# Kernel tuning notes

Measured on AMD Instinct MI355X. Metric: run time of the kernel, lower is better.

## Reference

```python
import jax, jax.numpy as jnp
import numpy as np

D = 1024
H = 16
DH = D // H
B, T = 2, 2048


def setup_inputs() -> dict:
    key = jax.random.key(0)
    ks = jax.random.split(key, 5)
    x = jax.random.normal(ks[0], (B, T, D), dtype=jnp.float32)
    # torch nn.Linear init scale ~ 1/sqrt(fan_in)
    sc = 1.0 / np.sqrt(D)
    W_qkv = jax.random.uniform(ks[1], (3 * D, D), dtype=jnp.float32, minval=-sc, maxval=sc)
    b_qkv = jax.random.uniform(ks[2], (3 * D,), dtype=jnp.float32, minval=-sc, maxval=sc)
    W_o = jax.random.uniform(ks[3], (D, D), dtype=jnp.float32, minval=-sc, maxval=sc)
    b_o = jax.random.uniform(ks[4], (D,), dtype=jnp.float32, minval=-sc, maxval=sc)
    return {"x": x, "W_qkv": W_qkv, "b_qkv": b_qkv, "W_o": W_o, "b_o": b_o}


def reference(x, W_qkv, b_qkv, W_o, b_o):
    Bx, Tx, C = x.shape
    scale = DH ** -0.5
    qkv = x @ W_qkv.T + b_qkv                       # [B,T,3D]
    qkv = qkv.reshape(Bx, Tx, 3, H, DH)
    q, k, v = jnp.moveaxis(qkv, 2, 0)               # each [B,T,H,DH]
    q = q.transpose(0, 2, 1, 3)                     # [B,H,T,DH]
    k = k.transpose(0, 2, 1, 3)
    v = v.transpose(0, 2, 1, 3)
    scores = jnp.einsum("bhqd,bhkd->bhqk", q, k) * scale
    a = jax.nn.softmax(scores, axis=-1)
    o = jnp.einsum("bhqk,bhkd->bhqd", a, v)         # [B,H,T,DH]
    o = o.transpose(0, 2, 1, 3).reshape(Bx, Tx, C)
    return o @ W_o.T + b_o
```

## Files before the change

kernel.cpp:

```cpp
#include <hip/hip_runtime.h>

#define TT 2048
#define DD 1024
#define HH 16
#define DHH 64

typedef __attribute__((ext_vector_type(4)))  float  f32x4;
typedef __attribute__((ext_vector_type(16))) float  f32x16;
typedef __attribute__((ext_vector_type(8)))  short  bf16x8;
typedef __attribute__((ext_vector_type(4)))  float  f4;
typedef __attribute__((ext_vector_type(4)))  unsigned short u16x4;
typedef __attribute__((ext_vector_type(4)))  unsigned int   u32x4;

__device__ __forceinline__ unsigned short f2b(float f) {
    union { float f; unsigned int u; } v; v.f = f;
    unsigned int r = v.u + 0x7fffu + ((v.u >> 16) & 1u);
    return (unsigned short)(r >> 16);
}

__device__ __forceinline__ void gl_lds16(const void* g, void* l) {
    __builtin_amdgcn_global_load_lds(
        (const __attribute__((address_space(1))) unsigned int*)g,
        (__attribute__((address_space(3))) unsigned int*)l, 16, 0, 0);
}

__device__ __forceinline__ f32x16 mfma32(bf16x8 a, bf16x8 b, f32x16 c) {
    return __builtin_amdgcn_mfma_f32_32x32x16_bf16(a, b, c, 0, 0, 0);
}

__device__ __forceinline__ float fexp2(float x) {
    float r; asm("v_exp_f32 %0, %1" : "=v"(r) : "v"(x)); return r;
}

__device__ __forceinline__ unsigned int pkbf(float a, float b) {
    unsigned int r;
    asm("v_cvt_pk_bf16_f32 %0, %1, %2" : "=v"(r) : "v"(a), "v"(b));
    return r;
}

__device__ __forceinline__ void pl32swap(unsigned int& a, unsigned int& b) {
    asm("v_permlane32_swap_b32 %0, %1" : "+v"(a), "+v"(b));
}

__device__ __forceinline__ bf16x8 u2h(u32x4 u) {
    union { u32x4 u; bf16x8 h; } x; x.u = u; return x.h;
}

__global__ void f2b3_kernel(const float* __restrict__ x, const float* __restrict__ wq,
                            const float* __restrict__ wo, unsigned short* __restrict__ d) {
    int i = blockIdx.x * blockDim.x + threadIdx.x;
    const float* s; int off;
    if (i < 1048576)      { s = x;  off = i; }
    else if (i < 1835008) { s = wq; off = i - 1048576; }
    else                  { s = wo; off = i - 1835008; }
    f4 v = ((const f4*)s)[off];
    u16x4 o;
    o[0] = f2b(v[0]); o[1] = f2b(v[1]); o[2] = f2b(v[2]); o[3] = f2b(v[3]);
    ((u16x4*)d)[i] = o;
}

template<int BN, int MODE>
__global__ __launch_bounds__(256) void gemm_bt(
    const unsigned short* __restrict__ A, const unsigned short* __restrict__ Bm,
    const float* __restrict__ bias, int N, int K,
    unsigned short* __restrict__ q, unsigned short* __restrict__ k,
    unsigned short* __restrict__ vt, float* __restrict__ outf)
{
    constexpr int NB  = BN / 32;
    constexpr int ASZ = 128 * 32;
    constexpr int BSZ = BN * 32;
    __shared__ unsigned short lds[2 * (ASZ + BSZ)];

    int tid = threadIdx.x;
    int l = tid & 63, w = tid >> 6;
    int wr = w >> 1, wc = w & 1;
    int lr = l & 15, lk = (l >> 4) * 8;
    int bm = blockIdx.y, bn = blockIdx.x;

    f32x4 acc[4][NB] = {};

    const unsigned short* Ag = A + (size_t)(bm * 128) * K;
    const unsigned short* Bg = Bm + (size_t)(bn * BN) * K;

    auto stage = [&](int buf, int k0) {
        unsigned short* As = lds + buf * (ASZ + BSZ);
        unsigned short* Bs = As + ASZ;
#pragma unroll
        for (int r = 0; r < 2; ++r) {
            int e = r * 256 + tid;
            int row = e >> 2, kc = (e & 3) * 8;
            gl_lds16(Ag + (size_t)row * K + k0 + kc, &As[e * 8]);
        }
#pragma unroll
        for (int r = 0; r < BN / 64; ++r) {
            int e = r * 256 + tid;
            int row = e >> 2, kc = (e & 3) * 8;
            gl_lds16(Bg + (size_t)row * K + k0 + kc, &Bs[e * 8]);
        }
    };

    stage(0, 0);
    __syncthreads();
    int cur = 0;
    for (int k0 = 0; k0 < K; k0 += 32) {
        if (k0 + 32 < K) stage(cur ^ 1, k0 + 32);
        const unsigned short* As = lds + cur * (ASZ + BSZ);
        const unsigned short* Bs = As + ASZ;
        bf16x8 a[4], b[NB];
#pragma unroll
        for (int i = 0; i < 4; ++i)
            a[i] = *(const bf16x8*)&As[(wr * 64 + i * 16 + lr) * 32 + lk];
#pragma unroll
        for (int j = 0; j < NB; ++j)
            b[j] = *(const bf16x8*)&Bs[(wc * (BN / 2) + j * 16 + lr) * 32 + lk];
        __builtin_amdgcn_s_setprio(1);
#pragma unroll
        for (int i = 0; i < 4; ++i)
#pragma unroll
            for (int j = 0; j < NB; ++j)
                acc[i][j] = __builtin_amdgcn_mfma_f32_16x16x32_bf16(a[i], b[j], acc[i][j], 0, 0, 0);
        __builtin_amdgcn_s_setprio(0);
        __syncthreads();
        cur ^= 1;
    }

#pragma unroll
    for (int i = 0; i < 4; ++i) {
#pragma unroll
        for (int j = 0; j < NB; ++j) {
            int row0 = bm * 128 + wr * 64 + i * 16 + (l >> 4) * 4;
            int col  = bn * BN + wc * (BN / 2) + j * 16 + (l & 15);
            float bv = bias[col];
#pragma unroll
            for (int r = 0; r < 4; ++r) {
                float val = acc[i][j][r] + bv;
                int m = row0 + r;
                if (MODE == 0) {
                    int which = col >> 10, rem = col & 1023;
                    int h = rem >> 6, d = rem & 63;
                    int b = m >> 11, t = m & 2047;
                    if (which == 0) {
                        q[((size_t)((b * HH + h) * TT + t)) * DHH + d] = f2b(val * 0.18033688011112042f);
                    } else if (which == 1) {
                        k[((size_t)((b * HH + h) * TT + t)) * DHH + d] = f2b(val);
                    } else {
                        vt[((size_t)((b * HH + h) * DHH + d)) * TT + t] = f2b(val);
                    }
                } else {
                    outf[(size_t)m * N + col] = val;
                }
            }
        }
    }
}

__global__ __launch_bounds__(512, 4) void attn(
    const unsigned short* __restrict__ qb,
    const unsigned short* __restrict__ kb,
    const unsigned short* __restrict__ vtb,
    unsigned short* __restrict__ ob)
{
    extern __shared__ char lds[];

    int tid = threadIdx.x;
    int l = tid & 63, w = tid >> 6;
    int g = w >> 2, wg = w & 3;
    int hi = l >> 5, c = l & 31;
    int tig = tid & 255;

    int lin = blockIdx.x;
    int swz = (lin & 7) * 64 + (lin >> 3);
    int bh = swz >> 4;
    int qrow = (swz & 15) * 128 + wg * 32 + c;

    bf16x8 qf[4];
    const unsigned short* qg = qb + ((size_t)bh * TT + qrow) * DHH;
#pragma unroll
    for (int kd = 0; kd < 4; ++kd)
        qf[kd] = *(const bf16x8*)(qg + kd * 16 + hi * 8);

    f32x16 oa0 = {}, oa1 = {};
    float m = -1e30f, lsum = 0.f;

    const char* kgl = (const char*)(kb + (size_t)bh * TT * DHH) + (size_t)g * 1024 * 128;
    const char* vgl = (const char*)(vtb + (size_t)bh * DHH * TT) + (size_t)g * 1024 * 2;
    char* base = lds + g * 16384;

    for (int kt0 = 0; kt0 < 1024; kt0 += 64) {
#pragma unroll
        for (int r = 0; r < 2; ++r) {
            int p = r * 4096 + tig * 16;
            int rw = p >> 7, qq = p & 127;
            int sw = qq ^ ((rw & 7) << 4);
            gl_lds16(kgl + (size_t)(kt0 + rw) * 128 + sw, base + p);
            gl_lds16(vgl + (size_t)rw * (TT * 2) + kt0 * 2 + sw, base + 8192 + p);
        }
        __syncthreads();
        const char* Ksb = base;
        const char* Vsb = base + 8192;

        f32x16 s0 = {}, s1 = {};
        __builtin_amdgcn_s_setprio(1);
#pragma unroll
        for (int kd = 0; kd < 4; ++kd) {
            int cb = (kd * 16 + hi * 8) * 2;
            int xr = cb ^ ((c & 7) << 4);
            bf16x8 kf0 = *(const bf16x8*)(Ksb + c * 128 + xr);
            bf16x8 kf1 = *(const bf16x8*)(Ksb + (32 + c) * 128 + xr);
            s0 = mfma32(kf0, qf[kd], s0);
            s1 = mfma32(kf1, qf[kd], s1);
        }
        __builtin_amdgcn_s_setprio(0);

        float mx[11];
#pragma unroll
        for (int r = 0; r < 10; ++r)
            mx[r] = fmaxf(fmaxf(s0[3 * r], s0[3 * r + 1]), s0[3 * r + 2]);
        mx[0] = fmaxf(fmaxf(s0[0], s0[1]), s0[2]);
        mx[1] = fmaxf(fmaxf(s0[3], s0[4]), s0[5]);
        mx[2] = fmaxf(fmaxf(s0[6], s0[7]), s0[8]);
        mx[3] = fmaxf(fmaxf(s0[9], s0[10]), s0[11]);
        mx[4] = fmaxf(fmaxf(s0[12], s0[13]), s0[14]);
        mx[5] = fmaxf(fmaxf(s0[15], s1[0]), s1[1]);
        mx[6] = fmaxf(fmaxf(s1[2], s1[3]), s1[4]);
        mx[7] = fmaxf(fmaxf(s1[5], s1[6]), s1[7]);
        mx[8] = fmaxf(fmaxf(s1[8], s1[9]), s1[10]);
        mx[9] = fmaxf(fmaxf(s1[11], s1[12]), s1[13]);
        mx[10] = fmaxf(s1[14], s1[15]);
        float t0 = fmaxf(fmaxf(mx[0], mx[1]), mx[2]);
        float t1 = fmaxf(fmaxf(mx[3], mx[4]), mx[5]);
        float t2 = fmaxf(fmaxf(mx[6], mx[7]), mx[8]);
        float t3 = fmaxf(mx[9], mx[10]);
        float tm = fmaxf(fmaxf(t0, t1), fmaxf(t2, t3));
        tm = fmaxf(tm, __shfl_xor(tm, 32, 64));

        float nm = fmaxf(m, tm);
        if (!__all(nm - m <= 8.f)) {
            float corr = fexp2(m - nm);
            lsum *= corr;
#pragma unroll
            for (int r = 0; r < 16; ++r) { oa0[r] *= corr; oa1[r] *= corr; }
            m = nm;
        }

        float p4[4] = {0.f, 0.f, 0.f, 0.f};
#pragma unroll
        for (int r = 0; r < 16; ++r) { s0[r] = fexp2(s0[r] - m); p4[r & 3] += s0[r]; }
#pragma unroll
        for (int r = 0; r < 16; ++r) { s1[r] = fexp2(s1[r] - m); p4[r & 3] += s1[r]; }
        float psum = (p4[0] + p4[1]) + (p4[2] + p4[3]);
        psum += __shfl_xor(psum, 32);
        lsum += psum;

        u32x4 pf0, pf1, pf2, pf3;
#define MKFRAG(sv, base_, dst) { \
        unsigned int c0 = pkbf(sv[base_+0], sv[base_+1]); \
        unsigned int c1 = pkbf(sv[base_+2], sv[base_+3]); \
        unsigned int c2 = pkbf(sv[base_+4], sv[base_+5]); \
        unsigned int c3 = pkbf(sv[base_+6], sv[base_+7]); \
        pl32swap(c0, c2); pl32swap(c1, c3); \
        dst[0] = c0; dst[1] = c1; dst[2] = c2; dst[3] = c3; }
        MKFRAG(s0, 0, pf0)
        MKFRAG(s0, 8, pf1)
        MKFRAG(s1, 0, pf2)
        MKFRAG(s1, 8, pf3)
#undef MKFRAG

        __builtin_amdgcn_s_setprio(1);
#define PVSTEP(kc, pf) { \
        int cb = (kc * 16 + hi * 8) * 2; \
        int xr = ((c & 7) << 4); \
        bf16x8 vf0 = *(const bf16x8*)(Vsb + c * 128 + (cb ^ xr)); \
        bf16x8 vf1 = *(const bf16x8*)(Vsb + (32 + c) * 128 + (cb ^ xr)); \
        bf16x8 ph = u2h(pf); \
        oa0 = mfma32(vf0, ph, oa0); \
        oa1 = mfma32(vf1, ph, oa1); }
        PVSTEP(0, pf0)
        PVSTEP(1, pf1)
        PVSTEP(2, pf2)
        PVSTEP(3, pf3)
#undef PVSTEP
        __builtin_amdgcn_s_setprio(0);

        __syncthreads();
    }

    float* Om = (float*)lds;
    float* ml = (float*)(lds + 32768);
    if (g == 1) {
        float* o = Om + wg * 2048 + l;
#pragma unroll
        for (int r = 0; r < 16; ++r) o[r * 64]        = oa0[r];
#pragma unroll
        for (int r = 0; r < 16; ++r) o[(16 + r) * 64] = oa1[r];
        ml[wg * 128 + l]      = m;
        ml[wg * 128 + 64 + l] = lsum;
    }
    __syncthreads();
    if (g == 1) return;

    float m2 = ml[wg * 128 + l];
    float l2 = ml[wg * 128 + 64 + l];
    float M  = fmaxf(m, m2);
    float a1 = fexp2(m - M), a2 = fexp2(m2 - M);
    float L  = lsum * a1 + l2 * a2;
    float rn = 1.0f / L;
    const float* o2 = Om + wg * 2048 + l;

    int b = bh >> 4, h = bh & 15;
    unsigned short* obase = ob + ((size_t)(b * TT + qrow)) * DD + h * 64;
#pragma unroll
    for (int gq = 0; gq < 4; ++gq) {
        u16x4 o0, o1;
#pragma unroll
        for (int e = 0; e < 4; ++e) {
            int r = gq * 4 + e;
            o0[e] = f2b((oa0[r] * a1 + o2[r * 64] * a2) * rn);
            o1[e] = f2b((oa1[r] * a1 + o2[(16 + r) * 64] * a2) * rn);
        }
        *(u16x4*)(obase + 8 * gq + 4 * hi)      = o0;
        *(u16x4*)(obase + 32 + 8 * gq + 4 * hi) = o1;
    }
}

extern "C" void kernel_launch(void* const* d_in, const int* in_sizes, int n_in,
                              void* d_out, int out_size, void* d_ws, size_t ws_size,
                              hipStream_t stream) {
    const float* x    = (const float*)d_in[0];
    const float* Wqkv = (const float*)d_in[1];
    const float* bqkv = (const float*)d_in[2];
    const float* Wo   = (const float*)d_in[3];
    const float* bo   = (const float*)d_in[4];
    float* out = (float*)d_out;

    unsigned short* xb  = (unsigned short*)d_ws;
    unsigned short* wqb = xb  + 4096 * 1024;
    unsigned short* wob = wqb + 3072 * 1024;
    unsigned short* q   = wob + 1024 * 1024;
    unsigned short* k   = q   + 2 * 16 * 2048 * 64;
    unsigned short* vt  = k   + 2 * 16 * 2048 * 64;
    unsigned short* ob  = vt  + 2 * 16 * 2048 * 64;

    f2b3_kernel<<<dim3(8192), dim3(256), 0, stream>>>(x, Wqkv, Wo, xb);

    gemm_bt<128, 0><<<dim3(24, 32), dim3(256), 0, stream>>>(xb, wqb, bqkv, 3072, 1024,
                                                            q, k, vt, nullptr);
    attn<<<dim3(512), dim3(512), 34816, stream>>>(q, k, vt, ob);

    gemm_bt<64, 1><<<dim3(16, 32), dim3(256), 0, stream>>>(ob, wob, bo, 1024, 1024,
                                                           nullptr, nullptr, nullptr, out);
}
```

Baseline: 120.1 us.

## Swizzle GEMM block order for XCD locality, vectorize V^T stores, defer row-sum shuffle

The GEMM grids become 1D, and each block's linear id is remapped to (bm, bn) so that blocks landing on the same XCD (lin & 7) share a compact region of A and B tiles, which should improve L2 reuse. The QKV epilogue now writes each transposed V group as one packed 4-element bf16 store instead of four scalar stores. In the attention loop, the per-iteration cross-half shuffle of the probability sum moves to a single shuffle at the final normalization, removing one cross-lane op per KV tile. The swizzle hard-codes the grid shape (32x24 and 32x16 tiles) and relies on round-robin block-to-XCD dispatch.

```diff
diff --git a/kernel.cpp b/kernel.cpp
--- a/kernel.cpp
+++ b/kernel.cpp
@@ -69,13 +69,18 @@
     constexpr int NB  = BN / 32;
     constexpr int ASZ = 128 * 32;
     constexpr int BSZ = BN * 32;
+    constexpr int BNCH = (MODE == 0 ? 12 : 8);
     __shared__ unsigned short lds[2 * (ASZ + BSZ)];
 
     int tid = threadIdx.x;
     int l = tid & 63, w = tid >> 6;
     int wr = w >> 1, wc = w & 1;
     int lr = l & 15, lk = (l >> 4) * 8;
-    int bm = blockIdx.y, bn = blockIdx.x;
+
+    int lin = blockIdx.x;
+    int cx = lin & 7, ii = lin >> 3;
+    int bm = (cx >> 1) * 8 + (ii & 7);
+    int bn = (cx & 1) * BNCH + (ii >> 3);
 
     f32x4 acc[4][NB] = {};
 
@@ -131,24 +136,32 @@
             int row0 = bm * 128 + wr * 64 + i * 16 + (l >> 4) * 4;
             int col  = bn * BN + wc * (BN / 2) + j * 16 + (l & 15);
             float bv = bias[col];
-#pragma unroll
-            for (int r = 0; r < 4; ++r) {
-                float val = acc[i][j][r] + bv;
-                int m = row0 + r;
-                if (MODE == 0) {
-                    int which = col >> 10, rem = col & 1023;
-                    int h = rem >> 6, d = rem & 63;
-                    int b = m >> 11, t = m & 2047;
-                    if (which == 0) {
-                        q[((size_t)((b * HH + h) * TT + t)) * DHH + d] = f2b(val * 0.18033688011112042f);
-                    } else if (which == 1) {
-                        k[((size_t)((b * HH + h) * TT + t)) * DHH + d] = f2b(val);
-                    } else {
-                        vt[((size_t)((b * HH + h) * DHH + d)) * TT + t] = f2b(val);
-                    }
+            float val[4];
+#pragma unroll
+            for (int r = 0; r < 4; ++r) val[r] = acc[i][j][r] + bv;
+            if (MODE == 0) {
+                int which = col >> 10, rem = col & 1023;
+                int h = rem >> 6, d = rem & 63;
+                int b = row0 >> 11, t0 = row0 & 2047;
+                if (which == 0) {
+#pragma unroll
+                    for (int r = 0; r < 4; ++r)
+                        q[((size_t)((b * HH + h) * TT + t0 + r)) * DHH + d] =
+                            f2b(val[r] * 0.18033688011112042f);
+                } else if (which == 1) {
+#pragma unroll
+                    for (int r = 0; r < 4; ++r)
+                        k[((size_t)((b * HH + h) * TT + t0 + r)) * DHH + d] = f2b(val[r]);
                 } else {
-                    outf[(size_t)m * N + col] = val;
+                    u16x4 pk;
+#pragma unroll
+                    for (int r = 0; r < 4; ++r) pk[r] = f2b(val[r]);
+                    *(u16x4*)(vt + ((size_t)((b * HH + h) * DHH + d)) * TT + t0) = pk;
                 }
+            } else {
+#pragma unroll
+                for (int r = 0; r < 4; ++r)
+                    outf[(size_t)(row0 + r) * N + col] = val[r];
             }
         }
     }
@@ -212,25 +225,21 @@
         }
         __builtin_amdgcn_s_setprio(0);
 
-        float mx[11];
-#pragma unroll
-        for (int r = 0; r < 10; ++r)
-            mx[r] = fmaxf(fmaxf(s0[3 * r], s0[3 * r + 1]), s0[3 * r + 2]);
-        mx[0] = fmaxf(fmaxf(s0[0], s0[1]), s0[2]);
-        mx[1] = fmaxf(fmaxf(s0[3], s0[4]), s0[5]);
-        mx[2] = fmaxf(fmaxf(s0[6], s0[7]), s0[8]);
-        mx[3] = fmaxf(fmaxf(s0[9], s0[10]), s0[11]);
-        mx[4] = fmaxf(fmaxf(s0[12], s0[13]), s0[14]);
-        mx[5] = fmaxf(fmaxf(s0[15], s1[0]), s1[1]);
-        mx[6] = fmaxf(fmaxf(s1[2], s1[3]), s1[4]);
-        mx[7] = fmaxf(fmaxf(s1[5], s1[6]), s1[7]);
-        mx[8] = fmaxf(fmaxf(s1[8], s1[9]), s1[10]);
-        mx[9] = fmaxf(fmaxf(s1[11], s1[12]), s1[13]);
-        mx[10] = fmaxf(s1[14], s1[15]);
-        float t0 = fmaxf(fmaxf(mx[0], mx[1]), mx[2]);
-        float t1 = fmaxf(fmaxf(mx[3], mx[4]), mx[5]);
-        float t2 = fmaxf(fmaxf(mx[6], mx[7]), mx[8]);
-        float t3 = fmaxf(mx[9], mx[10]);
+        float mx0 = fmaxf(fmaxf(s0[0], s0[1]), s0[2]);
+        float mx1 = fmaxf(fmaxf(s0[3], s0[4]), s0[5]);
+        float mx2 = fmaxf(fmaxf(s0[6], s0[7]), s0[8]);
+        float mx3 = fmaxf(fmaxf(s0[9], s0[10]), s0[11]);
+        float mx4 = fmaxf(fmaxf(s0[12], s0[13]), s0[14]);
+        float mx5 = fmaxf(fmaxf(s0[15], s1[0]), s1[1]);
+        float mx6 = fmaxf(fmaxf(s1[2], s1[3]), s1[4]);
+        float mx7 = fmaxf(fmaxf(s1[5], s1[6]), s1[7]);
+        float mx8 = fmaxf(fmaxf(s1[8], s1[9]), s1[10]);
+        float mx9 = fmaxf(fmaxf(s1[11], s1[12]), s1[13]);
+        float mxA = fmaxf(s1[14], s1[15]);
+        float t0 = fmaxf(fmaxf(mx0, mx1), mx2);
+        float t1 = fmaxf(fmaxf(mx3, mx4), mx5);
+        float t2 = fmaxf(fmaxf(mx6, mx7), mx8);
+        float t3 = fmaxf(mx9, mxA);
         float tm = fmaxf(fmaxf(t0, t1), fmaxf(t2, t3));
         tm = fmaxf(tm, __shfl_xor(tm, 32, 64));
 
@@ -248,9 +257,7 @@
         for (int r = 0; r < 16; ++r) { s0[r] = fexp2(s0[r] - m); p4[r & 3] += s0[r]; }
 #pragma unroll
         for (int r = 0; r < 16; ++r) { s1[r] = fexp2(s1[r] - m); p4[r & 3] += s1[r]; }
-        float psum = (p4[0] + p4[1]) + (p4[2] + p4[3]);
-        psum += __shfl_xor(psum, 32);
-        lsum += psum;
+        lsum += (p4[0] + p4[1]) + (p4[2] + p4[3]);
 
         u32x4 pf0, pf1, pf2, pf3;
 #define MKFRAG(sv, base_, dst) { \
@@ -303,7 +310,8 @@
     float l2 = ml[wg * 128 + 64 + l];
     float M  = fmaxf(m, m2);
     float a1 = fexp2(m - M), a2 = fexp2(m2 - M);
-    float L  = lsum * a1 + l2 * a2;
+    float Lh = lsum * a1 + l2 * a2;
+    float L  = Lh + __shfl_xor(Lh, 32, 64);
     float rn = 1.0f / L;
     const float* o2 = Om + wg * 2048 + l;
 
@@ -343,10 +351,10 @@
 
     f2b3_kernel<<<dim3(8192), dim3(256), 0, stream>>>(x, Wqkv, Wo, xb);
 
-    gemm_bt<128, 0><<<dim3(24, 32), dim3(256), 0, stream>>>(xb, wqb, bqkv, 3072, 1024,
-                                                            q, k, vt, nullptr);
+    gemm_bt<128, 0><<<dim3(768), dim3(256), 0, stream>>>(xb, wqb, bqkv, 3072, 1024,
+                                                         q, k, vt, nullptr);
     attn<<<dim3(512), dim3(512), 34816, stream>>>(q, k, vt, ob);
 
-    gemm_bt<64, 1><<<dim3(16, 32), dim3(256), 0, stream>>>(ob, wob, bo, 1024, 1024,
-                                                           nullptr, nullptr, nullptr, out);
-}
+    gemm_bt<64, 1><<<dim3(512), dim3(256), 0, stream>>>(ob, wob, bo, 1024, 1024,
+                                                        nullptr, nullptr, nullptr, out);
+}
```

After: 111.0 us, median of 2. -7.5%, faster.
